# Kernel optimization log

Hardware: AMD Instinct MI355X
Metric: run time of the kernel (lower is better)

Reference implementation:

```python
import jax, jax.numpy as jnp
import numpy as np

B, C, H, W = 4, 64, 128, 128
O = 64
K, S, P, D = 3, 1, 1, 1
K2 = K * K
Ho = (H + 2 * P - D * (K - 1) - 1) // S + 1
Wo = (W + 2 * P - D * (K - 1) - 1) // S + 1


def setup_inputs() -> dict:
    key = jax.random.key(0)
    k1, k2, k3, k4, k5 = jax.random.split(key, 5)
    x = jax.random.normal(k1, (B, C, H, W), dtype=jnp.float32)
    fan = C * K2
    # offset conv: out_channels = 2*n_offsets*K*K = 18; small init so offsets are ~O(1) px
    offset_w = jax.random.normal(k2, (2 * K2, C, K, K), dtype=jnp.float32) * (0.1 / np.sqrt(fan))
    offset_b = jax.random.normal(k3, (2 * K2,), dtype=jnp.float32) * 0.01
    deform_w = jax.random.normal(k4, (O, C, K, K), dtype=jnp.float32) * (1.0 / np.sqrt(fan))
    deform_b = jax.random.normal(k5, (O,), dtype=jnp.float32) * 0.01
    return {"x": x, "offset_w": offset_w, "offset_b": offset_b,
            "deform_w": deform_w, "deform_b": deform_b}


def _conv2d(x, w, b):
    y = jax.lax.conv_general_dilated(
        x, w, window_strides=(S, S), padding=[(P, P), (P, P)],
        rhs_dilation=(D, D), dimension_numbers=("NCHW", "OIHW", "NCHW"))
    return y + b[None, :, None, None]


def _gather(flat, iy, ix, h, w):
    # flat: [B, C, H*W]; iy/ix: [B, K2, Ho, Wo] int32
    valid = (iy >= 0) & (iy < h) & (ix >= 0) & (ix < w)
    idx = jnp.clip(iy, 0, h - 1) * w + jnp.clip(ix, 0, w - 1)
    b = flat.shape[0]
    v = jax.vmap(lambda f, i: f[:, i])(flat, idx.reshape(b, -1))  # [B, C, K2*Ho*Wo]
    v = v.reshape(b, flat.shape[1], *idx.shape[1:])               # [B, C, K2, Ho, Wo]
    return v * valid[:, None].astype(flat.dtype)


def _deform_conv(x, offset, w, b):
    # offset: [B, 2*K2, Ho, Wo] laid out as (dy, dx) pairs per kernel tap (torchvision order)
    off = offset.reshape(B, K2, 2, Ho, Wo)
    dy, dx = off[:, :, 0], off[:, :, 1]                           # [B, K2, Ho, Wo]
    ky = (jnp.arange(K2) // K * D).astype(jnp.float32)
    kx = (jnp.arange(K2) % K * D).astype(jnp.float32)
    base_y = (jnp.arange(Ho) * S - P).astype(jnp.float32)
    base_x = (jnp.arange(Wo) * S - P).astype(jnp.float32)
    py = dy + base_y[None, None, :, None] + ky[None, :, None, None]
    px = dx + base_x[None, None, None, :] + kx[None, :, None, None]

    y0 = jnp.floor(py); x0 = jnp.floor(px)
    wy = py - y0; wx = px - x0
    y0i = y0.astype(jnp.int32); x0i = x0.astype(jnp.int32)
    flat = x.reshape(B, C, H * W)
    w00 = ((1 - wy) * (1 - wx))[:, None]
    w01 = ((1 - wy) * wx)[:, None]
    w10 = (wy * (1 - wx))[:, None]
    w11 = (wy * wx)[:, None]
    sampled = (_gather(flat, y0i, x0i, H, W) * w00
               + _gather(flat, y0i, x0i + 1, H, W) * w01
               + _gather(flat, y0i + 1, x0i, H, W) * w10
               + _gather(flat, y0i + 1, x0i + 1, H, W) * w11)  # [B, C, K2, Ho, Wo]
    out = jnp.einsum("bckhw,ock->bohw", sampled, w.reshape(O, C, K2))
    return out + b[None, :, None, None]


def reference(x, offset_w, offset_b, deform_w, deform_b):
    offset = _conv2d(x, offset_w, offset_b)
    return _deform_conv(x, offset, deform_w, deform_b)
```

## Files before the change

kernel.cpp:

```cpp
#include <hip/hip_runtime.h>

#define BB 4
#define CC 64
#define HH 128
#define WW 128
#define OO 64
#define HWs (HH*WW)

typedef _Float16 f16;
typedef _Float16 f16x8 __attribute__((ext_vector_type(8)));
typedef float f32x4 __attribute__((ext_vector_type(4)));

__device__ __forceinline__ size_t xt_idx(int b, int y, int x) {
    return (((size_t)b * HH + y) * WW + x) * CC;
}

__global__ __launch_bounds__(256) void prep_all(const float* __restrict__ x,
                                                const float* __restrict__ offw,
                                                const float* __restrict__ dw,
                                                f16* __restrict__ xt,
                                                f16* __restrict__ wA_off,
                                                f16* __restrict__ wA_def) {
    const int bid = blockIdx.x;
    const int tid = threadIdx.x;
    if (bid < 512) {
        const int b = bid >> 7, y = bid & 127;
        const int px = tid & 127, half = tid >> 7;
        const float* src = x + (size_t)b * CC * HWs + (size_t)half * 32 * HWs + y * WW + px;
        f16* dst = xt + xt_idx(b, y, px) + half * 32;
        #pragma unroll
        for (int cg = 0; cg < 4; ++cg) {
            f16x8 v;
            #pragma unroll
            for (int j = 0; j < 8; ++j)
                v[j] = (f16)src[(size_t)(cg * 8 + j) * HWs];
            *(f16x8*)(dst + cg * 8) = v;
        }
    } else {
        const int t = (bid - 512) * 256 + tid;
        const int l = t & 63;
        const int idx = t >> 6;
        f16x8 v;
        if (idx < 36) {
            const int mt = idx & 1, ks = idx >> 1;
            const int o = mt * 16 + (l & 15);
            const int tap = ks >> 1, ky = tap / 3, kx = tap % 3;
            #pragma unroll
            for (int i = 0; i < 8; ++i) {
                const int c = (ks & 1) * 32 + (l >> 4) * 8 + i;
                v[i] = (o < 18) ? (f16)offw[((o * CC + c) * 3 + ky) * 3 + kx] : (f16)0.f;
            }
            *(f16x8*)(wA_off + (size_t)(idx * 64 + l) * 8) = v;
        } else if (idx < 108) {
            const int id2 = idx - 36;
            const int mt = id2 & 3, ks = (id2 >> 2) & 1, tap = id2 >> 3;
            const int o = mt * 16 + (l & 15);
            #pragma unroll
            for (int i = 0; i < 8; ++i) {
                const int c = ks * 32 + (l >> 4) * 8 + i;
                v[i] = (f16)dw[(size_t)(o * CC + c) * 9 + tap];
            }
            *(f16x8*)(wA_def + (size_t)(id2 * 64 + l) * 8) = v;
        }
    }
}

__device__ __forceinline__ f16x8 combine4(f16x8 p00, f16x8 p01, f16x8 p10, f16x8 p11,
                                          f16 h00, f16 h01, f16 h10, f16 h11) {
    const f16x8 W00 = {h00,h00,h00,h00,h00,h00,h00,h00};
    const f16x8 W01 = {h01,h01,h01,h01,h01,h01,h01,h01};
    const f16x8 W10 = {h10,h10,h10,h10,h10,h10,h10,h10};
    const f16x8 W11 = {h11,h11,h11,h11,h11,h11,h11,h11};
    return p00 * W00 + p01 * W01 + p10 * W10 + p11 * W11;
}

__global__ __launch_bounds__(128, 3) void deform_mfma(
    const f16* __restrict__ xt,
    const f16* __restrict__ wA_off,
    const float* __restrict__ offb,
    const f16* __restrict__ wA_def,
    const float* __restrict__ dbias,
    float* __restrict__ out)
{
    __shared__ __align__(16) char win[5 * 36 * 8 * 16];
    __shared__ float offs[18][32];

    const int tid = threadIdx.x;
    const int bid0 = blockIdx.x;
    const int bid = (bid0 & 7) * 256 + (bid0 >> 3);
    const int b = bid >> 9, row = (bid >> 2) & 127, px0 = (bid & 3) * 32;
    const int w = tid >> 6, l = tid & 63;
    const int pxs = l & 15, pxl = w * 16 + pxs, gpx = px0 + pxl, cg = l >> 4;

    for (int i = tid; i < 5 * 36 * 8; i += 128) {
        const int s = i / 288, rem = i - s * 288;
        const int xw = rem >> 3, ch8 = rem & 7;
        const int gy = row - 2 + s, gx = px0 - 2 + xw;
        f16x8 v = {};
        if (gy >= 0 && gy < HH && gx >= 0 && gx < WW)
            v = *(const f16x8*)(xt + xt_idx(b, gy, gx) + ch8 * 8);
        *(f16x8*)(win + ((s * 36 + xw) * 8 + (ch8 ^ ((xw + s) & 7))) * 16) = v;
    }
    __syncthreads();

    {
        f32x4 oa0 = {0,0,0,0}, oa1 = {0,0,0,0};
        #pragma unroll
        for (int ks = 0; ks < 18; ++ks) {
            const int tap = ks >> 1, chalf = ks & 1;
            const int ky = tap / 3, kx = tap - ky * 3;
            const int s = 1 + ky;
            const int xw = pxl + 1 + kx;
            const int ch8 = chalf * 4 + cg;
            const int byte = ((s * 36 + xw) * 8 + (ch8 ^ ((xw + s) & 7))) * 16;
            const f16x8 bf = *(const f16x8*)(win + byte);
            const f16x8 a0 = *(const f16x8*)(wA_off + (size_t)((ks * 2 + 0) * 64 + l) * 8);
            const f16x8 a1 = *(const f16x8*)(wA_off + (size_t)((ks * 2 + 1) * 64 + l) * 8);
            oa0 = __builtin_amdgcn_mfma_f32_16x16x32_f16(a0, bf, oa0, 0, 0, 0);
            oa1 = __builtin_amdgcn_mfma_f32_16x16x32_f16(a1, bf, oa1, 0, 0, 0);
        }
        #pragma unroll
        for (int reg = 0; reg < 4; ++reg) {
            const int o0 = cg * 4 + reg;
            offs[o0][pxl] = oa0[reg] + offb[o0];
            const int o1 = o0 + 16;
            if (o1 < 18) offs[o1][pxl] = oa1[reg] + offb[o1];
        }
    }
    __syncthreads();

    int o00[9], o01[9], o10[9], o11[9];
    f16 h00[9], h01[9], h10[9], h11[9];
    unsigned okm = 0;
    #pragma unroll
    for (int t = 0; t < 9; ++t) {
        const int ky = t / 3, kx = t - ky * 3;
        const float dy = offs[2 * t][pxl], dx = offs[2 * t + 1][pxl];
        const float py  = (float)(row - 1 + ky) + dy;
        const float pxf = (float)(gpx - 1 + kx) + dx;
        const float y0f = floorf(py), x0f = floorf(pxf);
        const float wy = py - y0f, wx = pxf - x0f;
        const int y0 = (int)y0f, x0 = (int)x0f;
        const int y1 = y0 + 1, x1 = x0 + 1;
        const bool vy0 = (y0 >= 0) & (y0 < HH), vy1 = (y1 >= 0) & (y1 < HH);
        const bool vx0 = (x0 >= 0) & (x0 < WW), vx1 = (x1 >= 0) & (x1 < WW);
        h00[t] = (f16)((1.f - wy) * (1.f - wx) * (float)(vy0 & vx0));
        h01[t] = (f16)((1.f - wy) * wx         * (float)(vy0 & vx1));
        h10[t] = (f16)(wy * (1.f - wx)         * (float)(vy1 & vx0));
        h11[t] = (f16)(wy * wx                 * (float)(vy1 & vx1));
        const int cy0 = min(max(y0, 0), HH - 1), cy1 = min(max(y1, 0), HH - 1);
        const int cx0 = min(max(x0, 0), WW - 1), cx1 = min(max(x1, 0), WW - 1);
        const int s0 = cy0 - (row - 2), s1 = cy1 - (row - 2);
        const int u0 = cx0 - (px0 - 2), u1 = cx1 - (px0 - 2);
        const int ok = (s0 >= 0) & (s0 < 5) & (s1 >= 0) & (s1 < 5) &
                       (u0 >= 0) & (u0 < 36) & (u1 >= 0) & (u1 < 36);
        if (__all(ok)) okm |= (1u << t);
        o00[t] = ((s0 * 36 + u0) * 8 + (cg ^ ((u0 + s0) & 7))) * 16;
        o01[t] = ((s0 * 36 + u1) * 8 + (cg ^ ((u1 + s0) & 7))) * 16;
        o10[t] = ((s1 * 36 + u0) * 8 + (cg ^ ((u0 + s1) & 7))) * 16;
        o11[t] = ((s1 * 36 + u1) * 8 + (cg ^ ((u1 + s1) & 7))) * 16;
    }

    f32x4 acc0 = {0,0,0,0}, acc1 = {0,0,0,0}, acc2 = {0,0,0,0}, acc3 = {0,0,0,0};

    #pragma unroll
    for (int t = 0; t < 9; ++t) {
        #pragma unroll
        for (int cpass = 0; cpass < 2; ++cpass) {
            const int flip = cpass << 6;
            f16x8 bf;
            if ((okm >> t) & 1) {
                const f16x8 p00 = *(const f16x8*)(win + (o00[t] ^ flip));
                const f16x8 p01 = *(const f16x8*)(win + (o01[t] ^ flip));
                const f16x8 p10 = *(const f16x8*)(win + (o10[t] ^ flip));
                const f16x8 p11 = *(const f16x8*)(win + (o11[t] ^ flip));
                bf = combine4(p00, p01, p10, p11, h00[t], h01[t], h10[t], h11[t]);
            } else {
                const int ky = t / 3, kx = t - ky * 3;
                const float dy = offs[2 * t][pxl], dx = offs[2 * t + 1][pxl];
                const float py  = (float)(row - 1 + ky) + dy;
                const float pxf = (float)(gpx - 1 + kx) + dx;
                const int y0 = (int)floorf(py), x0 = (int)floorf(pxf);
                const int cy0 = min(max(y0, 0), HH - 1), cy1 = min(max(y0 + 1, 0), HH - 1);
                const int cx0 = min(max(x0, 0), WW - 1), cx1 = min(max(x0 + 1, 0), WW - 1);
                const int ch8 = cpass * 4 + cg;
                const f16x8 p00 = *(const f16x8*)(xt + xt_idx(b, cy0, cx0) + ch8 * 8);
                const f16x8 p01 = *(const f16x8*)(xt + xt_idx(b, cy0, cx1) + ch8 * 8);
                const f16x8 p10 = *(const f16x8*)(xt + xt_idx(b, cy1, cx0) + ch8 * 8);
                const f16x8 p11 = *(const f16x8*)(xt + xt_idx(b, cy1, cx1) + ch8 * 8);
                bf = combine4(p00, p01, p10, p11, h00[t], h01[t], h10[t], h11[t]);
            }
            const f16* wa = wA_def + (size_t)(((t * 2 + cpass) * 4) * 64 + l) * 8;
            const f16x8 A0 = *(const f16x8*)(wa + (size_t)0 * 64 * 8);
            const f16x8 A1 = *(const f16x8*)(wa + (size_t)1 * 64 * 8);
            const f16x8 A2 = *(const f16x8*)(wa + (size_t)2 * 64 * 8);
            const f16x8 A3 = *(const f16x8*)(wa + (size_t)3 * 64 * 8);
            acc0 = __builtin_amdgcn_mfma_f32_16x16x32_f16(A0, bf, acc0, 0, 0, 0);
            acc1 = __builtin_amdgcn_mfma_f32_16x16x32_f16(A1, bf, acc1, 0, 0, 0);
            acc2 = __builtin_amdgcn_mfma_f32_16x16x32_f16(A2, bf, acc2, 0, 0, 0);
            acc3 = __builtin_amdgcn_mfma_f32_16x16x32_f16(A3, bf, acc3, 0, 0, 0);
        }
    }

    #pragma unroll
    for (int mt = 0; mt < 4; ++mt) {
        const f32x4 a = (mt == 0) ? acc0 : (mt == 1) ? acc1 : (mt == 2) ? acc2 : acc3;
        #pragma unroll
        for (int reg = 0; reg < 4; ++reg) {
            const int o = mt * 16 + cg * 4 + reg;
            out[(((size_t)b * OO + o) * HH + row) * WW + gpx] = a[reg] + dbias[o];
        }
    }
}

extern "C" void kernel_launch(void* const* d_in, const int* in_sizes, int n_in,
                              void* d_out, int out_size, void* d_ws, size_t ws_size,
                              hipStream_t stream) {
    const float* x     = (const float*)d_in[0];
    const float* offw  = (const float*)d_in[1];
    const float* offb  = (const float*)d_in[2];
    const float* dw    = (const float*)d_in[3];
    const float* dbias = (const float*)d_in[4];
    float* out = (float*)d_out;

    const size_t XT_BYTES    = (size_t)BB * HH * WW * CC * sizeof(f16);
    const size_t WAOFF_BYTES = 36 * 64 * 8 * sizeof(f16);

    f16* xt     = (f16*)d_ws;
    f16* wa_off = (f16*)((char*)d_ws + XT_BYTES);
    f16* wa_def = (f16*)((char*)d_ws + XT_BYTES + WAOFF_BYTES);
    (void)ws_size; (void)in_sizes; (void)n_in; (void)out_size;

    prep_all<<<512 + 27, 256, 0, stream>>>(x, offw, dw, xt, wa_off, wa_def);
    deform_mfma<<<BB * HH * 4, 128, 0, stream>>>(xt, wa_off, offb, wa_def, dbias, out);
}
```

Measured before the change: 43.64 us.

## Enlarge deform block to 4 rows, stage weights and taller window in LDS

Each block now handles 4 output rows by 32 pixels with 512 threads. Both weight matrices and a 9-row input window are staged in about 160KB of dynamic LDS, so the window halo is shared across rows and weights come from LDS instead of global memory. A fast path with no branches runs when every tap of a wave falls inside the window. The cost is a single block per CU, so little latency hiding, plus a large per-block weight preload repeated across 512 blocks.

```diff
diff --git a/kernel.cpp b/kernel.cpp
--- a/kernel.cpp
+++ b/kernel.cpp
@@ -6,9 +6,12 @@
 #define WW 128
 #define OO 64
 #define HWs (HH*WW)
+#define R9 9
+#define XW 37
 
 typedef _Float16 f16;
 typedef _Float16 f16x8 __attribute__((ext_vector_type(8)));
+typedef _Float16 f16x2 __attribute__((ext_vector_type(2)));
 typedef float f32x4 __attribute__((ext_vector_type(4)));
 
 __device__ __forceinline__ size_t xt_idx(int b, int y, int x) {
@@ -74,7 +77,7 @@
     return p00 * W00 + p01 * W01 + p10 * W10 + p11 * W11;
 }
 
-__global__ __launch_bounds__(128, 3) void deform_mfma(
+__global__ __launch_bounds__(512) void deform_mfma(
     const f16* __restrict__ xt,
     const f16* __restrict__ wA_off,
     const float* __restrict__ offb,
@@ -82,24 +85,51 @@
     const float* __restrict__ dbias,
     float* __restrict__ out)
 {
-    __shared__ __align__(16) char win[5 * 36 * 8 * 16];
-    __shared__ float offs[18][32];
+    extern __shared__ __align__(16) char lds[];
+    char*  wdef_l = lds;
+    char*  woff_l = lds + 73728;
+    char*  winp   = lds + 110592;
+    float* offs   = (float*)(lds + 153216);
 
     const int tid = threadIdx.x;
     const int bid0 = blockIdx.x;
-    const int bid = (bid0 & 7) * 256 + (bid0 >> 3);
-    const int b = bid >> 9, row = (bid >> 2) & 127, px0 = (bid & 3) * 32;
-    const int w = tid >> 6, l = tid & 63;
-    const int pxs = l & 15, pxl = w * 16 + pxs, gpx = px0 + pxl, cg = l >> 4;
-
-    for (int i = tid; i < 5 * 36 * 8; i += 128) {
-        const int s = i / 288, rem = i - s * 288;
-        const int xw = rem >> 3, ch8 = rem & 7;
-        const int gy = row - 2 + s, gx = px0 - 2 + xw;
-        f16x8 v = {};
-        if (gy >= 0 && gy < HH && gx >= 0 && gx < WW)
-            v = *(const f16x8*)(xt + xt_idx(b, gy, gx) + ch8 * 8);
-        *(f16x8*)(win + ((s * 36 + xw) * 8 + (ch8 ^ ((xw + s) & 7))) * 16) = v;
+    const int bid = (bid0 & 7) * 64 + (bid0 >> 3);
+    const int b  = bid >> 7;
+    const int rg = (bid >> 2) & 31;
+    const int pg = bid & 3;
+    const int r0 = rg * 4, px0 = pg * 32;
+
+    const int wid = tid >> 6, l = tid & 63;
+    const int ri = wid >> 1, pt = wid & 1;
+    const int pxs = l & 15, cg = l >> 4;
+    const int pxl = pt * 16 + pxs;
+    const int row = r0 + ri;
+    const int gpx = px0 + pxl;
+    const int slot = ri * 32 + pxl;
+
+    #pragma unroll
+    for (int it = 0; it < 9; ++it) {
+        const int i = tid + it * 512;
+        *(f16x8*)(wdef_l + i * 16) = *(const f16x8*)((const char*)wA_def + (size_t)i * 16);
+    }
+    #pragma unroll
+    for (int it = 0; it < 5; ++it) {
+        const int i = tid + it * 512;
+        if (i < 2304)
+            *(f16x8*)(woff_l + i * 16) = *(const f16x8*)((const char*)wA_off + (size_t)i * 16);
+    }
+    #pragma unroll
+    for (int it = 0; it < 6; ++it) {
+        const int i = tid + it * 512;
+        if (i < R9 * XW * 8) {
+            const int s = i / (XW * 8), rem = i - s * (XW * 8);
+            const int xw = rem >> 3, ch8 = rem & 7;
+            const int gy = r0 - 2 + s, gx = px0 - 2 + xw;
+            f16x8 v = {};
+            if (gy >= 0 && gy < HH && gx >= 0 && gx < WW)
+                v = *(const f16x8*)(xt + xt_idx(b, gy, gx) + ch8 * 8);
+            *(f16x8*)(winp + ((s * XW + xw) * 8 + (ch8 ^ ((xw + s) & 7))) * 16) = v;
+        }
     }
     __syncthreads();
 
@@ -109,33 +139,32 @@
         for (int ks = 0; ks < 18; ++ks) {
             const int tap = ks >> 1, chalf = ks & 1;
             const int ky = tap / 3, kx = tap - ky * 3;
-            const int s = 1 + ky;
+            const int s = ri + 1 + ky;
             const int xw = pxl + 1 + kx;
             const int ch8 = chalf * 4 + cg;
-            const int byte = ((s * 36 + xw) * 8 + (ch8 ^ ((xw + s) & 7))) * 16;
-            const f16x8 bf = *(const f16x8*)(win + byte);
-            const f16x8 a0 = *(const f16x8*)(wA_off + (size_t)((ks * 2 + 0) * 64 + l) * 8);
-            const f16x8 a1 = *(const f16x8*)(wA_off + (size_t)((ks * 2 + 1) * 64 + l) * 8);
+            const f16x8 bf = *(const f16x8*)(winp + ((s * XW + xw) * 8 + (ch8 ^ ((xw + s) & 7))) * 16);
+            const f16x8 a0 = *(const f16x8*)(woff_l + ((ks * 2 + 0) * 64 + l) * 16);
+            const f16x8 a1 = *(const f16x8*)(woff_l + ((ks * 2 + 1) * 64 + l) * 16);
             oa0 = __builtin_amdgcn_mfma_f32_16x16x32_f16(a0, bf, oa0, 0, 0, 0);
             oa1 = __builtin_amdgcn_mfma_f32_16x16x32_f16(a1, bf, oa1, 0, 0, 0);
         }
         #pragma unroll
         for (int reg = 0; reg < 4; ++reg) {
-            const int o0 = cg * 4 + reg;
-            offs[o0][pxl] = oa0[reg] + offb[o0];
-            const int o1 = o0 + 16;
-            if (o1 < 18) offs[o1][pxl] = oa1[reg] + offb[o1];
+            const int c0 = cg * 4 + reg;
+            offs[c0 * 128 + slot] = oa0[reg] + offb[c0];
+            const int c1 = c0 + 16;
+            if (c1 < 18) offs[c1 * 128 + slot] = oa1[reg] + offb[c1];
         }
     }
     __syncthreads();
 
     int o00[9], o01[9], o10[9], o11[9];
-    f16 h00[9], h01[9], h10[9], h11[9];
+    f16x2 hA[9], hB[9];
     unsigned okm = 0;
     #pragma unroll
     for (int t = 0; t < 9; ++t) {
         const int ky = t / 3, kx = t - ky * 3;
-        const float dy = offs[2 * t][pxl], dx = offs[2 * t + 1][pxl];
+        const float dy = offs[(2 * t) * 128 + slot], dx = offs[(2 * t + 1) * 128 + slot];
         const float py  = (float)(row - 1 + ky) + dy;
         const float pxf = (float)(gpx - 1 + kx) + dx;
         const float y0f = floorf(py), x0f = floorf(pxf);
@@ -144,61 +173,79 @@
         const int y1 = y0 + 1, x1 = x0 + 1;
         const bool vy0 = (y0 >= 0) & (y0 < HH), vy1 = (y1 >= 0) & (y1 < HH);
         const bool vx0 = (x0 >= 0) & (x0 < WW), vx1 = (x1 >= 0) & (x1 < WW);
-        h00[t] = (f16)((1.f - wy) * (1.f - wx) * (float)(vy0 & vx0));
-        h01[t] = (f16)((1.f - wy) * wx         * (float)(vy0 & vx1));
-        h10[t] = (f16)(wy * (1.f - wx)         * (float)(vy1 & vx0));
-        h11[t] = (f16)(wy * wx                 * (float)(vy1 & vx1));
+        hA[t][0] = (f16)((1.f - wy) * (1.f - wx) * (float)(vy0 & vx0));
+        hA[t][1] = (f16)((1.f - wy) * wx         * (float)(vy0 & vx1));
+        hB[t][0] = (f16)(wy * (1.f - wx)         * (float)(vy1 & vx0));
+        hB[t][1] = (f16)(wy * wx                 * (float)(vy1 & vx1));
         const int cy0 = min(max(y0, 0), HH - 1), cy1 = min(max(y1, 0), HH - 1);
         const int cx0 = min(max(x0, 0), WW - 1), cx1 = min(max(x1, 0), WW - 1);
-        const int s0 = cy0 - (row - 2), s1 = cy1 - (row - 2);
+        const int s0 = cy0 - (r0 - 2), s1 = cy1 - (r0 - 2);
         const int u0 = cx0 - (px0 - 2), u1 = cx1 - (px0 - 2);
-        const int ok = (s0 >= 0) & (s0 < 5) & (s1 >= 0) & (s1 < 5) &
-                       (u0 >= 0) & (u0 < 36) & (u1 >= 0) & (u1 < 36);
+        const int ok = (s0 >= 0) & (s0 < R9) & (s1 >= 0) & (s1 < R9) &
+                       (u0 >= 0) & (u0 < XW) & (u1 >= 0) & (u1 < XW);
         if (__all(ok)) okm |= (1u << t);
-        o00[t] = ((s0 * 36 + u0) * 8 + (cg ^ ((u0 + s0) & 7))) * 16;
-        o01[t] = ((s0 * 36 + u1) * 8 + (cg ^ ((u1 + s0) & 7))) * 16;
-        o10[t] = ((s1 * 36 + u0) * 8 + (cg ^ ((u0 + s1) & 7))) * 16;
-        o11[t] = ((s1 * 36 + u1) * 8 + (cg ^ ((u1 + s1) & 7))) * 16;
+        const int s0c = min(max(s0, 0), R9 - 1), s1c = min(max(s1, 0), R9 - 1);
+        const int u0c = min(max(u0, 0), XW - 1), u1c = min(max(u1, 0), XW - 1);
+        o00[t] = ((s0c * XW + u0c) * 8 + (cg ^ ((u0c + s0c) & 7))) * 16;
+        o01[t] = ((s0c * XW + u1c) * 8 + (cg ^ ((u1c + s0c) & 7))) * 16;
+        o10[t] = ((s1c * XW + u0c) * 8 + (cg ^ ((u0c + s1c) & 7))) * 16;
+        o11[t] = ((s1c * XW + u1c) * 8 + (cg ^ ((u1c + s1c) & 7))) * 16;
     }
 
     f32x4 acc0 = {0,0,0,0}, acc1 = {0,0,0,0}, acc2 = {0,0,0,0}, acc3 = {0,0,0,0};
 
-    #pragma unroll
-    for (int t = 0; t < 9; ++t) {
-        #pragma unroll
-        for (int cpass = 0; cpass < 2; ++cpass) {
-            const int flip = cpass << 6;
-            f16x8 bf;
-            if ((okm >> t) & 1) {
-                const f16x8 p00 = *(const f16x8*)(win + (o00[t] ^ flip));
-                const f16x8 p01 = *(const f16x8*)(win + (o01[t] ^ flip));
-                const f16x8 p10 = *(const f16x8*)(win + (o10[t] ^ flip));
-                const f16x8 p11 = *(const f16x8*)(win + (o11[t] ^ flip));
-                bf = combine4(p00, p01, p10, p11, h00[t], h01[t], h10[t], h11[t]);
-            } else {
-                const int ky = t / 3, kx = t - ky * 3;
-                const float dy = offs[2 * t][pxl], dx = offs[2 * t + 1][pxl];
-                const float py  = (float)(row - 1 + ky) + dy;
-                const float pxf = (float)(gpx - 1 + kx) + dx;
-                const int y0 = (int)floorf(py), x0 = (int)floorf(pxf);
-                const int cy0 = min(max(y0, 0), HH - 1), cy1 = min(max(y0 + 1, 0), HH - 1);
-                const int cx0 = min(max(x0, 0), WW - 1), cx1 = min(max(x0 + 1, 0), WW - 1);
-                const int ch8 = cpass * 4 + cg;
-                const f16x8 p00 = *(const f16x8*)(xt + xt_idx(b, cy0, cx0) + ch8 * 8);
-                const f16x8 p01 = *(const f16x8*)(xt + xt_idx(b, cy0, cx1) + ch8 * 8);
-                const f16x8 p10 = *(const f16x8*)(xt + xt_idx(b, cy1, cx0) + ch8 * 8);
-                const f16x8 p11 = *(const f16x8*)(xt + xt_idx(b, cy1, cx1) + ch8 * 8);
-                bf = combine4(p00, p01, p10, p11, h00[t], h01[t], h10[t], h11[t]);
+    if (okm == 0x1FFu) {
+        #pragma unroll
+        for (int j = 0; j < 18; ++j) {
+            const int t = j >> 1, fl = (j & 1) << 6;
+            const f16x8 p00 = *(const f16x8*)(winp + (o00[t] ^ fl));
+            const f16x8 p01 = *(const f16x8*)(winp + (o01[t] ^ fl));
+            const f16x8 p10 = *(const f16x8*)(winp + (o10[t] ^ fl));
+            const f16x8 p11 = *(const f16x8*)(winp + (o11[t] ^ fl));
+            const f16x8 bf = combine4(p00, p01, p10, p11,
+                                      hA[t][0], hA[t][1], hB[t][0], hB[t][1]);
+            const char* wa = wdef_l + ((j * 4) * 64 + l) * 16;
+            acc0 = __builtin_amdgcn_mfma_f32_16x16x32_f16(*(const f16x8*)(wa + 0 * 1024), bf, acc0, 0, 0, 0);
+            acc1 = __builtin_amdgcn_mfma_f32_16x16x32_f16(*(const f16x8*)(wa + 1 * 1024), bf, acc1, 0, 0, 0);
+            acc2 = __builtin_amdgcn_mfma_f32_16x16x32_f16(*(const f16x8*)(wa + 2 * 1024), bf, acc2, 0, 0, 0);
+            acc3 = __builtin_amdgcn_mfma_f32_16x16x32_f16(*(const f16x8*)(wa + 3 * 1024), bf, acc3, 0, 0, 0);
+        }
+    } else {
+        #pragma unroll
+        for (int t = 0; t < 9; ++t) {
+            #pragma unroll
+            for (int cpass = 0; cpass < 2; ++cpass) {
+                const int flip = cpass << 6;
+                f16x8 bf;
+                if ((okm >> t) & 1) {
+                    const f16x8 p00 = *(const f16x8*)(winp + (o00[t] ^ flip));
+                    const f16x8 p01 = *(const f16x8*)(winp + (o01[t] ^ flip));
+                    const f16x8 p10 = *(const f16x8*)(winp + (o10[t] ^ flip));
+                    const f16x8 p11 = *(const f16x8*)(winp + (o11[t] ^ flip));
+                    bf = combine4(p00, p01, p10, p11,
+                                  hA[t][0], hA[t][1], hB[t][0], hB[t][1]);
+                } else {
+                    const int ky = t / 3, kx = t - ky * 3;
+                    const float dy = offs[(2 * t) * 128 + slot], dx = offs[(2 * t + 1) * 128 + slot];
+                    const float py  = (float)(row - 1 + ky) + dy;
+                    const float pxf = (float)(gpx - 1 + kx) + dx;
+                    const int y0 = (int)floorf(py), x0 = (int)floorf(pxf);
+                    const int cy0 = min(max(y0, 0), HH - 1), cy1 = min(max(y0 + 1, 0), HH - 1);
+                    const int cx0 = min(max(x0, 0), WW - 1), cx1 = min(max(x0 + 1, 0), WW - 1);
+                    const int ch8 = cpass * 4 + cg;
+                    const f16x8 p00 = *(const f16x8*)(xt + xt_idx(b, cy0, cx0) + ch8 * 8);
+                    const f16x8 p01 = *(const f16x8*)(xt + xt_idx(b, cy0, cx1) + ch8 * 8);
+                    const f16x8 p10 = *(const f16x8*)(xt + xt_idx(b, cy1, cx0) + ch8 * 8);
+                    const f16x8 p11 = *(const f16x8*)(xt + xt_idx(b, cy1, cx1) + ch8 * 8);
+                    bf = combine4(p00, p01, p10, p11,
+                                  hA[t][0], hA[t][1], hB[t][0], hB[t][1]);
+                }
+                const char* wa = wdef_l + (((t * 2 + cpass) * 4) * 64 + l) * 16;
+                acc0 = __builtin_amdgcn_mfma_f32_16x16x32_f16(*(const f16x8*)(wa + 0 * 1024), bf, acc0, 0, 0, 0);
+                acc1 = __builtin_amdgcn_mfma_f32_16x16x32_f16(*(const f16x8*)(wa + 1 * 1024), bf, acc1, 0, 0, 0);
+                acc2 = __builtin_amdgcn_mfma_f32_16x16x32_f16(*(const f16x8*)(wa + 2 * 1024), bf, acc2, 0, 0, 0);
+                acc3 = __builtin_amdgcn_mfma_f32_16x16x32_f16(*(const f16x8*)(wa + 3 * 1024), bf, acc3, 0, 0, 0);
             }
-            const f16* wa = wA_def + (size_t)(((t * 2 + cpass) * 4) * 64 + l) * 8;
-            const f16x8 A0 = *(const f16x8*)(wa + (size_t)0 * 64 * 8);
-            const f16x8 A1 = *(const f16x8*)(wa + (size_t)1 * 64 * 8);
-            const f16x8 A2 = *(const f16x8*)(wa + (size_t)2 * 64 * 8);
-            const f16x8 A3 = *(const f16x8*)(wa + (size_t)3 * 64 * 8);
-            acc0 = __builtin_amdgcn_mfma_f32_16x16x32_f16(A0, bf, acc0, 0, 0, 0);
-            acc1 = __builtin_amdgcn_mfma_f32_16x16x32_f16(A1, bf, acc1, 0, 0, 0);
-            acc2 = __builtin_amdgcn_mfma_f32_16x16x32_f16(A2, bf, acc2, 0, 0, 0);
-            acc3 = __builtin_amdgcn_mfma_f32_16x16x32_f16(A3, bf, acc3, 0, 0, 0);
         }
     }
 
@@ -231,6 +278,10 @@
     f16* wa_def = (f16*)((char*)d_ws + XT_BYTES + WAOFF_BYTES);
     (void)ws_size; (void)in_sizes; (void)n_in; (void)out_size;
 
+    const int LDS_BYTES = 162432;
+    (void)hipFuncSetAttribute((const void*)deform_mfma,
+                              hipFuncAttributeMaxDynamicSharedMemorySize, LDS_BYTES);
+
     prep_all<<<512 + 27, 256, 0, stream>>>(x, offw, dw, xt, wa_off, wa_def);
-    deform_mfma<<<BB * HH * 4, 128, 0, stream>>>(xt, wa_off, offb, wa_def, dbias, out);
-}
+    deform_mfma<<<512, 512, LDS_BYTES, stream>>>(xt, wa_off, offb, wa_def, dbias, out);
+}
```

After: 39.40 us. 9.7% less time.
